# Kernel optimization log

Measured on AMD Instinct MI355X. Metric: run time of the kernel, lower is better.

Reference implementation:

```python
import math
import jax, jax.numpy as jnp
import numpy as np

N_FLOWS = 5
DIM = 64
NH = 128          # hidden multiplier -> hidden width = DIM*NH = 8192
BATCH = 4096


def _masks(out_f, in_f, dim):
    od, idd = out_f // dim, in_f // dim
    mask_d = np.zeros((out_f, in_f), np.float32)
    mask_o = np.ones((out_f, in_f), np.float32)
    for i in range(dim):
        mask_d[i * od:(i + 1) * od, i * idd:(i + 1) * idd] = 1.0
        mask_o[i * od:(i + 1) * od, i * idd:] = 0.0
    return jnp.asarray(mask_d), jnp.asarray(mask_o)

MASK_D1, MASK_O1 = _masks(DIM * NH, DIM, DIM)   # layer 1: (H, D)
MASK_D2, MASK_O2 = _masks(DIM, DIM * NH, DIM)   # layer 2: (D, H)


def masked_weight(x, W, dw, b, mask_d, mask_o, dim, grad=None):
    """MaskedWeight.forward. W:(out,in), dw:(out,1), b:(out,)."""
    out_f, in_f = W.shape
    od, idd = out_f // dim, in_f // dim
    w = jnp.exp(W) * mask_d + W * mask_o                 # (out, in)
    wsn = jnp.sum(w * w, axis=-1, keepdims=True)         # (out, 1)
    wn = jnp.exp(dw) * w / jnp.sqrt(wsn)                 # weight-normalized
    wpl = dw + W - 0.5 * jnp.log(wsn)                    # (out, in)
    # extract diagonal blocks of wpl^T: (dim, idd, od)
    blocks = wpl.reshape(dim, od, dim, idd)
    wpl_t = blocks[np.arange(dim), :, np.arange(dim), :].transpose(0, 2, 1)
    y = x @ wn.T + b                                     # (B, out)
    g = wpl_t.transpose(0, 2, 1)                         # (dim, od, idd)
    if grad is None:
        new_grad = jnp.broadcast_to(g[None], (x.shape[0],) + g.shape)
    else:
        # logsumexp over contracted block axis: out (B, dim, od, b_prev)
        new_grad = jax.nn.logsumexp(
            g[None, :, :, None, :] + jnp.swapaxes(grad, -2, -1)[:, :, None, :, :],
            axis=-1)
    return y, new_grad


def tanh_layer(x, grad):
    g = -2.0 * (x - math.log(2.0) + jax.nn.softplus(-2.0 * x))
    return jnp.tanh(x), g.reshape(grad.shape) + grad


def bnaf_flow(x, W1, d1, b1, W2, d2, b2, gate):
    h, g = masked_weight(x, W1, d1, b1, MASK_D1, MASK_O1, DIM)
    h, g = tanh_layer(h, g)
    y, g = masked_weight(h, W2, d2, b2, MASK_D2, MASK_O2, DIM, grad=g)
    grad = g[:, :, 0, 0]                                  # (B, DIM) -- squeeze
    if gate is None:                                      # res=None (last flow)
        return y, jnp.sum(grad, axis=-1)
    s = jax.nn.sigmoid(gate)                              # res='gated'
    out = s * y + (1.0 - s) * x
    ld = jnp.sum(jax.nn.softplus(grad + gate) - jax.nn.softplus(gate), axis=-1)
    return out, ld


def setup_inputs() -> dict:
    key = jax.random.key(0)
    ks = jax.random.split(key, 8)
    H = DIM * NH
    return {
        "x":  jax.random.normal(ks[0], (BATCH, DIM), jnp.float32),
        "W1": jax.random.normal(ks[1], (N_FLOWS, H, DIM), jnp.float32) * 0.1,
        "d1": jax.random.normal(ks[2], (N_FLOWS, H, 1), jnp.float32) * 0.1,
        "b1": jax.random.normal(ks[3], (N_FLOWS, H), jnp.float32) * 0.01,
        "W2": jax.random.normal(ks[4], (N_FLOWS, DIM, H), jnp.float32) * 0.1,
        "d2": jax.random.normal(ks[5], (N_FLOWS, DIM, 1), jnp.float32) * 0.1,
        "b2": jax.random.normal(ks[6], (N_FLOWS, DIM), jnp.float32) * 0.01,
        "gates": jax.random.normal(ks[7], (N_FLOWS - 1,), jnp.float32),
    }


def reference(x, W1, d1, b1, W2, d2, b2, gates):
    log_det = jnp.zeros(x.shape[0], x.dtype)
    for f in range(N_FLOWS):
        gate = gates[f] if f < N_FLOWS - 1 else None
        x, ld = bnaf_flow(x, W1[f], d1[f], b1[f], W2[f], d2[f], b2[f], gate)
        log_det = log_det + ld
        if f < N_FLOWS - 1:                               # Permutation 'flip'
            x = x[:, ::-1]
    return x, log_det
```

## Files before the change

kernel.cpp:

```cpp
#include <hip/hip_runtime.h>
#include <hip/hip_bf16.h>
#include <math.h>

#define NFLOWS 5
#define DIMF 64
#define HID 8192
#define BATCHN 4096

typedef unsigned int u32;
typedef __bf16 bf16x8 __attribute__((ext_vector_type(8)));
typedef float f32x4 __attribute__((ext_vector_type(4)));

__device__ __forceinline__ short f2bf_s(float x){
  u32 b = __float_as_uint(x);
  b += 0x7fff + ((b >> 16) & 1);
  return (short)(b >> 16);
}
__device__ __forceinline__ u32 pk_bf16(float a, float b){
#if __has_builtin(__builtin_amdgcn_cvt_pk_bf16_f32)
  typedef __bf16 bf16x2_t __attribute__((ext_vector_type(2)));
  bf16x2_t r = __builtin_amdgcn_cvt_pk_bf16_f32(a, b);
  return __builtin_bit_cast(u32, r);
#else
  u32 x = __float_as_uint(a); x += 0x7fff + ((x >> 16) & 1);
  u32 y = __float_as_uint(b); y += 0x7fff + ((y >> 16) & 1);
  return (x >> 16) | (y & 0xffff0000u);
#endif
}
__device__ __forceinline__ float softplus_f(float z){
  return fmaxf(z, 0.f) + log1pf(__expf(-fabsf(z)));
}

__global__ __launch_bounds__(1024) void prep_fused_kernel(
    const float* __restrict__ W1, const float* __restrict__ d1,
    const float* __restrict__ W2, const float* __restrict__ d2,
    short* __restrict__ wn1s, short* __restrict__ wn2s,
    float* __restrict__ expc4, float* __restrict__ cmax)
{
  __shared__ float g1s[128];
  __shared__ float cbuf[128];
  __shared__ float red[16];
  __shared__ float Msh;

  const int tid  = threadIdx.x;
  const int w    = tid >> 6;
  const int lane = tid & 63;
  const int f    = blockIdx.x >> 6;
  const int i    = blockIdx.x & 63;

  {
    const int ks2 = lane >> 5, q = (lane & 31) >> 3, j = lane & 7;
    #pragma unroll
    for (int it = 0; it < 8; ++it) {
      int rr = w * 8 + it;
      size_t R = (size_t)(f * HID + i * 128 + rr);
      float Wv = W1[R * 64 + lane];
      float wv = (lane == i) ? __expf(Wv) : ((lane < i) ? Wv : 0.f);
      float sq = wv * wv;
      #pragma unroll
      for (int m = 1; m < 64; m <<= 1) sq += __shfl_xor(sq, m, 64);
      float d1v = d1[R];
      float sc = __expf(d1v) * rsqrtf(sq);
      int nt = rr >> 4, n16 = rr & 15;
      size_t dst = ((((size_t)(f * 64 + i) * 8 + nt) * 2 + ks2) << 9)
                 + ((q * 16 + n16) << 3) + j;
      wn1s[dst] = f2bf_s(wv * sc);
      if (lane == i) g1s[rr] = d1v + Wv - 0.5f * __logf(sq);
    }
  }
  __syncthreads();

  const float* Wrow = W2 + ((size_t)(f * DIMF + i)) * HID;
  const float d2v = d2[f * DIMF + i];
  const int k0 = tid * 8;
  const int kb = tid >> 4;
  float4 a = *(const float4*)(Wrow + k0);
  float4 b = *(const float4*)(Wrow + k0 + 4);
  float wv[8] = {a.x, a.y, a.z, a.w, b.x, b.y, b.z, b.w};
  const bool diag = (kb == i);
  float cv[8];
  float mv[8];
  #pragma unroll
  for (int e = 0; e < 8; ++e) {
    if (diag)        { cv[e] = g1s[(k0 - i * 128) + e] + d2v + wv[e]; mv[e] = __expf(wv[e]); }
    else if (kb > i) { mv[e] = 0.f; }
    else             { mv[e] = wv[e]; }
  }
  float part = 0.f;
  #pragma unroll
  for (int e = 0; e < 8; ++e) part = fmaf(mv[e], mv[e], part);
  #pragma unroll
  for (int m = 1; m < 64; m <<= 1) part += __shfl_xor(part, m, 64);
  if (lane == 0) red[w] = part;
  __syncthreads();
  float wsn = 0.f;
  #pragma unroll
  for (int e = 0; e < 16; ++e) wsn += red[e];
  float ls = __logf(wsn);
  float sc2 = __expf(d2v) * rsqrtf(wsn);

  if (diag) {
    int rr0 = k0 - i * 128;
    #pragma unroll
    for (int e = 0; e < 8; ++e) cbuf[rr0 + e] = cv[e] - 0.5f * ls;
  }
  {
    int ks = (k0 >> 5) & 3, qq = (k0 >> 3) & 3;
    int mt2 = i >> 4, c16r = i & 15;
    size_t dst = ((((size_t)(f * 64 + kb) * 4 + ks) * 4 + mt2) << 9)
               + ((qq * 16 + c16r) << 3);
    uint4 pk4;
    pk4.x = pk_bf16(mv[0]*sc2, mv[1]*sc2); pk4.y = pk_bf16(mv[2]*sc2, mv[3]*sc2);
    pk4.z = pk_bf16(mv[4]*sc2, mv[5]*sc2); pk4.w = pk_bf16(mv[6]*sc2, mv[7]*sc2);
    *(uint4*)(wn2s + dst) = pk4;
  }
  __syncthreads();

  if (w == 0) {
    float m = fmaxf(cbuf[lane], cbuf[lane + 64]);
    #pragma unroll
    for (int s = 1; s < 64; s <<= 1) m = fmaxf(m, __shfl_xor(m, s, 64));
    if (lane == 0) { cmax[f * DIMF + i] = m; Msh = m; }
  }
  __syncthreads();
  if (tid < 128) expc4[f * HID + i * 128 + tid] = 4.f * __expf(cbuf[tid] - Msh);
}

__global__ __launch_bounds__(1024, 4)
void bnaf_main_kernel(
    const float* __restrict__ x_in,
    const float* __restrict__ b1, const float* __restrict__ b2,
    const float* __restrict__ gates,
    const short* __restrict__ wn1s,
    const short* __restrict__ wn2s,
    const float* __restrict__ expc4, const float* __restrict__ cmax,
    float* __restrict__ out)
{
  __shared__ __attribute__((aligned(16))) char smem[146816];
  float* xs  = (float*)smem;
  short* xbS = (short*)(smem + 4352);
  float* ldp = (float*)(smem + 145792);

  const int tid  = threadIdx.x;
  const int w    = tid >> 6;
  const int lane = tid & 63;
  const int c16  = lane & 15;
  const int q    = lane >> 4;
  const int r0   = blockIdx.x * 16;

  short* tbuf0 = (short*)(smem + 6528 + w * 8704);
  short* tbuf1 = (short*)(smem + 6528 + w * 8704 + 4352);

  {
    int row = tid >> 6, col = tid & 63;
    float v = x_in[((size_t)(r0 + row) << 6) | col];
    xs[row * 68 + col] = v;
    xbS[(col >> 3) * 136 + row * 8 + (col & 7)] = f2bf_s(v);
  }
  float ldtot = 0.f;
  __syncthreads();

  #pragma unroll 1
  for (int f = 0; f < NFLOWS; ++f) {
    const float gatev = (f < NFLOWS - 1) ? gates[f] : 0.f;
    const float spg   = (f < NFLOWS - 1) ? softplus_f(gatev) : 0.f;

    const bf16x8 xa0 = *(const bf16x8*)(xbS + q * 136 + c16 * 8);
    const bf16x8 xa1 = *(const bf16x8*)(xbS + (4 + q) * 136 + c16 * 8);

    f32x4 yacc[4];
    #pragma unroll
    for (int n = 0; n < 4; ++n) yacc[n] = f32x4{0.f, 0.f, 0.f, 0.f};
    float ldacc = 0.f;

    #pragma unroll 1
    for (int ii = 0; ii < 4; ++ii) {
      const int i = ii * 16 + w;
      short* tb = (ii & 1) ? tbuf1 : tbuf0;
      const short* p1l = wn1s + (((size_t)(f * 64 + i)) << 13) + lane * 8;
      const float* b1p = b1    + f * HID + i * 128 + q * 4;
      const float* ecp = expc4 + f * HID + i * 128 + q * 4;
      const bool hiHalf = (i >= 32);

      float s0 = 0.f, s1 = 0.f;
      f32x4 dd[4];

      #pragma unroll
      for (int nt = 0; nt < 4; ++nt) {
        float4 b1q = *(const float4*)(b1p + nt * 16);
        f32x4 z = {b1q.x, b1q.y, b1q.z, b1q.w};
        bf16x8 bw0 = *(const bf16x8*)(p1l + nt * 1024);
        dd[nt] = __builtin_amdgcn_mfma_f32_16x16x32_bf16(bw0, xa0, z, 0, 0, 0);
      }
      if (hiHalf) {
        #pragma unroll
        for (int nt = 0; nt < 4; ++nt) {
          bf16x8 bw1 = *(const bf16x8*)(p1l + nt * 1024 + 512);
          dd[nt] = __builtin_amdgcn_mfma_f32_16x16x32_bf16(bw1, xa1, dd[nt], 0, 0, 0);
        }
      }
      #pragma unroll
      for (int nt = 0; nt < 4; ++nt) {
        float4 ecq = *(const float4*)(ecp + nt * 16);
        float t[4];
        #pragma unroll
        for (int r = 0; r < 4; ++r) {
          float ee = (r == 0) ? ecq.x : (r == 1) ? ecq.y : (r == 2) ? ecq.z : ecq.w;
          float h  = dd[nt][r];
          float up = __expf(-2.f * fabsf(h));
          float vp = __builtin_amdgcn_rcpf(1.f + up);
          float ta = fmaf(-2.f * up, vp, 1.f);
          t[r] = copysignf(ta, h);
          float c1 = ee * up, c2 = vp * vp;
          if (r & 1) s1 = fmaf(c1, c2, s1); else s0 = fmaf(c1, c2, s0);
        }
        uint2 pk; pk.x = pk_bf16(t[0], t[1]); pk.y = pk_bf16(t[2], t[3]);
        *(uint2*)(tb + c16 * 136 + nt * 16 + q * 4) = pk;
      }

      if (ii > 0) {
        const int ip = i - 16;
        short* tp = ((ii - 1) & 1) ? tbuf1 : tbuf0;
        __builtin_amdgcn_sched_barrier(0);
        asm volatile("s_waitcnt lgkmcnt(0)" ::: "memory");
        const short* p2l = wn2s + (((size_t)(f * 64 + ip)) << 13) + lane * 8;
        const int mt0 = ip >> 4;
        #pragma unroll
        for (int ks = 0; ks < 4; ++ks) {
          if (ks == 2) __builtin_amdgcn_sched_barrier(0);
          bf16x8 tfrag = *(const bf16x8*)(tp + c16 * 136 + ks * 32 + q * 8);
          #pragma unroll
          for (int mt = 0; mt < 4; ++mt) {
            if (mt >= mt0) {
              bf16x8 wb = *(const bf16x8*)(p2l + (ks * 4 + mt) * 512);
              yacc[mt] = __builtin_amdgcn_mfma_f32_16x16x32_bf16(wb, tfrag, yacc[mt], 0, 0, 0);
            }
          }
        }
        __builtin_amdgcn_sched_barrier(0);
      }

      #pragma unroll
      for (int nt = 0; nt < 4; ++nt) {
        float4 b1q = *(const float4*)(b1p + (nt + 4) * 16);
        f32x4 z = {b1q.x, b1q.y, b1q.z, b1q.w};
        bf16x8 bw0 = *(const bf16x8*)(p1l + (nt + 4) * 1024);
        dd[nt] = __builtin_amdgcn_mfma_f32_16x16x32_bf16(bw0, xa0, z, 0, 0, 0);
      }
      if (hiHalf) {
        #pragma unroll
        for (int nt = 0; nt < 4; ++nt) {
          bf16x8 bw1 = *(const bf16x8*)(p1l + (nt + 4) * 1024 + 512);
          dd[nt] = __builtin_amdgcn_mfma_f32_16x16x32_bf16(bw1, xa1, dd[nt], 0, 0, 0);
        }
      }
      #pragma unroll
      for (int nt = 0; nt < 4; ++nt) {
        float4 ecq = *(const float4*)(ecp + (nt + 4) * 16);
        float t[4];
        #pragma unroll
        for (int r = 0; r < 4; ++r) {
          float ee = (r == 0) ? ecq.x : (r == 1) ? ecq.y : (r == 2) ? ecq.z : ecq.w;
          float h  = dd[nt][r];
          float up = __expf(-2.f * fabsf(h));
          float vp = __builtin_amdgcn_rcpf(1.f + up);
          float ta = fmaf(-2.f * up, vp, 1.f);
          t[r] = copysignf(ta, h);
          float c1 = ee * up, c2 = vp * vp;
          if (r & 1) s1 = fmaf(c1, c2, s1); else s0 = fmaf(c1, c2, s0);
        }
        uint2 pk; pk.x = pk_bf16(t[0], t[1]); pk.y = pk_bf16(t[2], t[3]);
        *(uint2*)(tb + c16 * 136 + (nt + 4) * 16 + q * 4) = pk;
      }

      float sacc = s0 + s1;
      sacc += __shfl_xor(sacc, 16, 64);
      sacc += __shfl_xor(sacc, 32, 64);
      const float Mi = cmax[f * DIMF + i];
      float grad = Mi + __logf(sacc);
      ldacc += (f < NFLOWS - 1) ? (softplus_f(grad + gatev) - spg) : grad;
    }

    {
      const int ip = 48 + w;
      __builtin_amdgcn_sched_barrier(0);
      asm volatile("s_waitcnt lgkmcnt(0)" ::: "memory");
      const short* p2l = wn2s + (((size_t)(f * 64 + ip)) << 13) + lane * 8;
      const int mt0 = ip >> 4;
      #pragma unroll
      for (int ks = 0; ks < 4; ++ks) {
        if (ks == 2) __builtin_amdgcn_sched_barrier(0);
        bf16x8 tfrag = *(const bf16x8*)(tbuf1 + c16 * 136 + ks * 32 + q * 8);
        #pragma unroll
        for (int mt = 0; mt < 4; ++mt) {
          if (mt >= mt0) {
            bf16x8 wb = *(const bf16x8*)(p2l + (ks * 4 + mt) * 512);
            yacc[mt] = __builtin_amdgcn_mfma_f32_16x16x32_bf16(wb, tfrag, yacc[mt], 0, 0, 0);
          }
        }
      }
      __builtin_amdgcn_sched_barrier(0);
    }

    float* ypw = (float*)(smem + 6528 + w * 8704);
    #pragma unroll
    for (int mt = 0; mt < 4; ++mt)
      #pragma unroll
      for (int r = 0; r < 4; ++r)
        ypw[(mt * 4 + r) * 65 + lane] = yacc[mt][r];
    if (q == 0) ldp[w * 16 + c16] = ldacc;
    __syncthreads();

    float sgate = 0.f;
    if (f < NFLOWS - 1) sgate = __builtin_amdgcn_rcpf(1.f + __expf(-gatev));
    int row = tid >> 6, col = tid & 63;
    int idx = ((col >> 4) * 4 + (col & 3)) * 65 + (((col >> 2) & 3) * 16 + row);
    float v = b2[f * DIMF + col];
    #pragma unroll
    for (int ww = 0; ww < 16; ++ww)
      v += ((const float*)(smem + 6528 + ww * 8704))[idx];
    float nx = 0.f; int nrow = 0, ncol = 0;
    if (f < NFLOWS - 1) {
      float xv = xs[row * 68 + col];
      nx = fmaf(sgate, v - xv, xv);
      nrow = row; ncol = 63 - col;
    } else {
      out[((size_t)(r0 + row) << 6) | col] = v;
    }
    if (tid < 16) {
      float a = 0.f;
      #pragma unroll
      for (int ww = 0; ww < 16; ++ww) a += ldp[ww * 16 + tid];
      ldtot += a;
    }
    __syncthreads();
    if (f < NFLOWS - 1) {
      xs[nrow * 68 + ncol] = nx;
      xbS[(ncol >> 3) * 136 + nrow * 8 + (ncol & 7)] = f2bf_s(nx);
      __syncthreads();
    }
  }

  if (tid < 16) out[(size_t)BATCHN * DIMF + r0 + tid] = ldtot;
}

extern "C" void kernel_launch(void* const* d_in, const int* in_sizes, int n_in,
                              void* d_out, int out_size, void* d_ws, size_t ws_size,
                              hipStream_t stream)
{
  const float* x     = (const float*)d_in[0];
  const float* W1    = (const float*)d_in[1];
  const float* d1    = (const float*)d_in[2];
  const float* b1    = (const float*)d_in[3];
  const float* W2    = (const float*)d_in[4];
  const float* d2    = (const float*)d_in[5];
  const float* b2    = (const float*)d_in[6];
  const float* gates = (const float*)d_in[7];
  float* out = (float*)d_out;

  char* ws = (char*)d_ws;
  short* wn1s  = (short*)ws;
  short* wn2s  = (short*)(ws + 5242880);
  float* expc4 = (float*)(ws + 10485760);
  float* cmaxp = (float*)(ws + 10649600);

  hipLaunchKernelGGL(prep_fused_kernel, dim3(320), dim3(1024), 0, stream,
                     W1, d1, W2, d2, wn1s, wn2s, expc4, cmaxp);
  hipLaunchKernelGGL(bnaf_main_kernel, dim3(256), dim3(1024), 0, stream,
                     x, b1, b2, gates, wn1s, wn2s, expc4, cmaxp, out);
}
```

Measured before the change: 266.0 us.

## Fuse weight prep and main flow into one cooperative kernel with grid syncs

Merges the weight-normalization prep kernel and the main flow kernel into a single cooperative launch over 256 blocks. Two grid.sync barriers replace the kernel boundary. The prep work is redistributed: each wave handles 10 rows of W1 and one W2 row, and the per-row g1 values go through a new global scratch buffer instead of shared memory. This removes one launch and the gap between kernels, but adds grid-barrier cost, reads W2 twice, and makes prep run on fewer waves (320 of 4096) in the second phase.

```diff
diff --git a/kernel.cpp b/kernel.cpp
--- a/kernel.cpp
+++ b/kernel.cpp
@@ -1,6 +1,9 @@
 #include <hip/hip_runtime.h>
 #include <hip/hip_bf16.h>
+#include <hip/hip_cooperative_groups.h>
 #include <math.h>
+
+namespace cg = cooperative_groups;
 
 #define NFLOWS 5
 #define DIMF 64
@@ -31,30 +34,37 @@
   return fmaxf(z, 0.f) + log1pf(__expf(-fabsf(z)));
 }
 
-__global__ __launch_bounds__(1024) void prep_fused_kernel(
+__global__ __launch_bounds__(1024, 4)
+void bnaf_coop_kernel(
+    const float* __restrict__ x_in,
     const float* __restrict__ W1, const float* __restrict__ d1,
+    const float* __restrict__ b1,
     const float* __restrict__ W2, const float* __restrict__ d2,
+    const float* __restrict__ b2, const float* __restrict__ gates,
     short* __restrict__ wn1s, short* __restrict__ wn2s,
-    float* __restrict__ expc4, float* __restrict__ cmax)
+    float* __restrict__ expc4, float* __restrict__ cmax,
+    float* __restrict__ g1, float* __restrict__ out)
 {
-  __shared__ float g1s[128];
-  __shared__ float cbuf[128];
-  __shared__ float red[16];
-  __shared__ float Msh;
+  cg::grid_group grid = cg::this_grid();
+
+  __shared__ __attribute__((aligned(16))) char smem[146816];
+  float* xs  = (float*)smem;
+  short* xbS = (short*)(smem + 4352);
+  float* ldp = (float*)(smem + 145792);
 
   const int tid  = threadIdx.x;
   const int w    = tid >> 6;
   const int lane = tid & 63;
-  const int f    = blockIdx.x >> 6;
-  const int i    = blockIdx.x & 63;
 
   {
-    const int ks2 = lane >> 5, q = (lane & 31) >> 3, j = lane & 7;
+    const int gw = blockIdx.x * 16 + w;
+    const int ks2 = lane >> 5, q4 = (lane & 31) >> 3, j = lane & 7;
     #pragma unroll
-    for (int it = 0; it < 8; ++it) {
-      int rr = w * 8 + it;
-      size_t R = (size_t)(f * HID + i * 128 + rr);
-      float Wv = W1[R * 64 + lane];
+    for (int it = 0; it < 10; ++it) {
+      int R = gw * 10 + it;
+      int f = R >> 13, rl = R & (HID - 1);
+      int i = rl >> 7, rr = rl & 127;
+      float Wv = W1[(size_t)R * 64 + lane];
       float wv = (lane == i) ? __expf(Wv) : ((lane < i) ? Wv : 0.f);
       float sq = wv * wv;
       #pragma unroll
@@ -63,87 +73,91 @@
       float sc = __expf(d1v) * rsqrtf(sq);
       int nt = rr >> 4, n16 = rr & 15;
       size_t dst = ((((size_t)(f * 64 + i) * 8 + nt) * 2 + ks2) << 9)
-                 + ((q * 16 + n16) << 3) + j;
+                 + ((q4 * 16 + n16) << 3) + j;
       wn1s[dst] = f2bf_s(wv * sc);
-      if (lane == i) g1s[rr] = d1v + Wv - 0.5f * __logf(sq);
+      if (lane == i) g1[R] = d1v + Wv - 0.5f * __logf(sq);
     }
   }
-  __syncthreads();
-
-  const float* Wrow = W2 + ((size_t)(f * DIMF + i)) * HID;
-  const float d2v = d2[f * DIMF + i];
-  const int k0 = tid * 8;
-  const int kb = tid >> 4;
-  float4 a = *(const float4*)(Wrow + k0);
-  float4 b = *(const float4*)(Wrow + k0 + 4);
-  float wv[8] = {a.x, a.y, a.z, a.w, b.x, b.y, b.z, b.w};
-  const bool diag = (kb == i);
-  float cv[8];
-  float mv[8];
-  #pragma unroll
-  for (int e = 0; e < 8; ++e) {
-    if (diag)        { cv[e] = g1s[(k0 - i * 128) + e] + d2v + wv[e]; mv[e] = __expf(wv[e]); }
-    else if (kb > i) { mv[e] = 0.f; }
-    else             { mv[e] = wv[e]; }
+  grid.sync();
+
+  {
+    const int gw = blockIdx.x * 16 + w;
+    if (gw < 320) {
+      const int f = gw >> 6, i = gw & 63;
+      const float* Wrow = W2 + ((size_t)(f * DIMF + i)) * HID;
+      const float d2v = d2[f * DIMF + i];
+      float part = 0.f;
+      #pragma unroll
+      for (int e = 0; e < 16; ++e) {
+        int k0 = e * 512 + lane * 8;
+        int kb = k0 >> 7;
+        float4 a = *(const float4*)(Wrow + k0);
+        float4 b = *(const float4*)(Wrow + k0 + 4);
+        float wv[8] = {a.x, a.y, a.z, a.w, b.x, b.y, b.z, b.w};
+        if (kb == i) {
+          #pragma unroll
+          for (int e2 = 0; e2 < 8; ++e2) wv[e2] = __expf(wv[e2]);
+        } else if (kb > i) {
+          #pragma unroll
+          for (int e2 = 0; e2 < 8; ++e2) wv[e2] = 0.f;
+        }
+        #pragma unroll
+        for (int e2 = 0; e2 < 8; ++e2) part = fmaf(wv[e2], wv[e2], part);
+      }
+      #pragma unroll
+      for (int m = 1; m < 64; m <<= 1) part += __shfl_xor(part, m, 64);
+      float ls = __logf(part);
+      float sc2 = __expf(d2v) * rsqrtf(part);
+
+      const int mt2 = i >> 4, c16r = i & 15;
+      float cv[8];
+      float lm = -1e30f;
+      #pragma unroll
+      for (int e = 0; e < 16; ++e) {
+        int k0 = e * 512 + lane * 8;
+        int kb = k0 >> 7;
+        float4 a = *(const float4*)(Wrow + k0);
+        float4 b = *(const float4*)(Wrow + k0 + 4);
+        float wv[8] = {a.x, a.y, a.z, a.w, b.x, b.y, b.z, b.w};
+        if (kb == i) {
+          float4 ga = *(const float4*)(g1 + f * HID + k0);
+          float4 gb = *(const float4*)(g1 + f * HID + k0 + 4);
+          float gg[8] = {ga.x, ga.y, ga.z, ga.w, gb.x, gb.y, gb.z, gb.w};
+          #pragma unroll
+          for (int e2 = 0; e2 < 8; ++e2) {
+            cv[e2] = gg[e2] + d2v + wv[e2] - 0.5f * ls;
+            lm = fmaxf(lm, cv[e2]);
+            wv[e2] = __expf(wv[e2]);
+          }
+        } else if (kb > i) {
+          #pragma unroll
+          for (int e2 = 0; e2 < 8; ++e2) wv[e2] = 0.f;
+        }
+        int ks = (k0 >> 5) & 3, qq = (k0 >> 3) & 3;
+        size_t dst = ((((size_t)(f * 64 + kb) * 4 + ks) * 4 + mt2) << 9)
+                   + ((qq * 16 + c16r) << 3);
+        uint4 pk4;
+        pk4.x = pk_bf16(wv[0]*sc2, wv[1]*sc2); pk4.y = pk_bf16(wv[2]*sc2, wv[3]*sc2);
+        pk4.z = pk_bf16(wv[4]*sc2, wv[5]*sc2); pk4.w = pk_bf16(wv[6]*sc2, wv[7]*sc2);
+        *(uint4*)(wn2s + dst) = pk4;
+      }
+      #pragma unroll
+      for (int m = 1; m < 64; m <<= 1) lm = fmaxf(lm, __shfl_xor(lm, m, 64));
+      if ((lane >> 4) == (i & 3)) {
+        int base = f * HID + i * 128 + (lane & 15) * 8;
+        float4 ea, eb;
+        ea.x = 4.f*__expf(cv[0]-lm); ea.y = 4.f*__expf(cv[1]-lm);
+        ea.z = 4.f*__expf(cv[2]-lm); ea.w = 4.f*__expf(cv[3]-lm);
+        eb.x = 4.f*__expf(cv[4]-lm); eb.y = 4.f*__expf(cv[5]-lm);
+        eb.z = 4.f*__expf(cv[6]-lm); eb.w = 4.f*__expf(cv[7]-lm);
+        *(float4*)(expc4 + base)     = ea;
+        *(float4*)(expc4 + base + 4) = eb;
+      }
+      if (lane == 0) cmax[f * DIMF + i] = lm;
+    }
   }
-  float part = 0.f;
-  #pragma unroll
-  for (int e = 0; e < 8; ++e) part = fmaf(mv[e], mv[e], part);
-  #pragma unroll
-  for (int m = 1; m < 64; m <<= 1) part += __shfl_xor(part, m, 64);
-  if (lane == 0) red[w] = part;
-  __syncthreads();
-  float wsn = 0.f;
-  #pragma unroll
-  for (int e = 0; e < 16; ++e) wsn += red[e];
-  float ls = __logf(wsn);
-  float sc2 = __expf(d2v) * rsqrtf(wsn);
-
-  if (diag) {
-    int rr0 = k0 - i * 128;
-    #pragma unroll
-    for (int e = 0; e < 8; ++e) cbuf[rr0 + e] = cv[e] - 0.5f * ls;
-  }
-  {
-    int ks = (k0 >> 5) & 3, qq = (k0 >> 3) & 3;
-    int mt2 = i >> 4, c16r = i & 15;
-    size_t dst = ((((size_t)(f * 64 + kb) * 4 + ks) * 4 + mt2) << 9)
-               + ((qq * 16 + c16r) << 3);
-    uint4 pk4;
-    pk4.x = pk_bf16(mv[0]*sc2, mv[1]*sc2); pk4.y = pk_bf16(mv[2]*sc2, mv[3]*sc2);
-    pk4.z = pk_bf16(mv[4]*sc2, mv[5]*sc2); pk4.w = pk_bf16(mv[6]*sc2, mv[7]*sc2);
-    *(uint4*)(wn2s + dst) = pk4;
-  }
-  __syncthreads();
-
-  if (w == 0) {
-    float m = fmaxf(cbuf[lane], cbuf[lane + 64]);
-    #pragma unroll
-    for (int s = 1; s < 64; s <<= 1) m = fmaxf(m, __shfl_xor(m, s, 64));
-    if (lane == 0) { cmax[f * DIMF + i] = m; Msh = m; }
-  }
-  __syncthreads();
-  if (tid < 128) expc4[f * HID + i * 128 + tid] = 4.f * __expf(cbuf[tid] - Msh);
-}
-
-__global__ __launch_bounds__(1024, 4)
-void bnaf_main_kernel(
-    const float* __restrict__ x_in,
-    const float* __restrict__ b1, const float* __restrict__ b2,
-    const float* __restrict__ gates,
-    const short* __restrict__ wn1s,
-    const short* __restrict__ wn2s,
-    const float* __restrict__ expc4, const float* __restrict__ cmax,
-    float* __restrict__ out)
-{
-  __shared__ __attribute__((aligned(16))) char smem[146816];
-  float* xs  = (float*)smem;
-  short* xbS = (short*)(smem + 4352);
-  float* ldp = (float*)(smem + 145792);
-
-  const int tid  = threadIdx.x;
-  const int w    = tid >> 6;
-  const int lane = tid & 63;
+  grid.sync();
+
   const int c16  = lane & 15;
   const int q    = lane >> 4;
   const int r0   = blockIdx.x * 16;
@@ -363,9 +377,14 @@
   short* wn2s  = (short*)(ws + 5242880);
   float* expc4 = (float*)(ws + 10485760);
   float* cmaxp = (float*)(ws + 10649600);
-
-  hipLaunchKernelGGL(prep_fused_kernel, dim3(320), dim3(1024), 0, stream,
-                     W1, d1, W2, d2, wn1s, wn2s, expc4, cmaxp);
-  hipLaunchKernelGGL(bnaf_main_kernel, dim3(256), dim3(1024), 0, stream,
-                     x, b1, b2, gates, wn1s, wn2s, expc4, cmaxp, out);
-}
+  float* g1    = (float*)(ws + 10650880);
+
+  void* args[] = {
+    (void*)&x, (void*)&W1, (void*)&d1, (void*)&b1,
+    (void*)&W2, (void*)&d2, (void*)&b2, (void*)&gates,
+    (void*)&wn1s, (void*)&wn2s, (void*)&expc4, (void*)&cmaxp,
+    (void*)&g1, (void*)&out
+  };
+  hipLaunchCooperativeKernel((const void*)bnaf_coop_kernel,
+                             dim3(256), dim3(1024), args, 0, stream);
+}
```

New measurement: 467.0 us. 1.76x slower.
